# Kernel tuning notes

Hardware: AMD Instinct MI355X
Metric: run time of the kernel (lower is better)

The kernel has to match this reference:

```python
import jax, jax.numpy as jnp
import numpy as np
import math

H = 1024      # hidden_size
NH = 16       # num_heads
HD = H // NH  # head_dim
B, S = 4, 2048

def setup_inputs() -> dict:
    key = jax.random.key(0)
    ks = jax.random.split(key, 10)
    sc = 1.0 / math.sqrt(H)
    return {
        "hidden_states": jax.random.normal(ks[0], (B, S, H), dtype=jnp.float32),
        "attention_mask": jnp.ones((B, S), dtype=jnp.int32),
        "Wq": jax.random.normal(ks[1], (H, H), dtype=jnp.float32) * sc,
        "bq": jnp.zeros((H,), dtype=jnp.float32),
        "Wk": jax.random.normal(ks[2], (H, H), dtype=jnp.float32) * sc,
        "bk": jnp.zeros((H,), dtype=jnp.float32),
        "Wv": jax.random.normal(ks[3], (H, H), dtype=jnp.float32) * sc,
        "bv": jnp.zeros((H,), dtype=jnp.float32),
        "Wo": jax.random.normal(ks[4], (H, H), dtype=jnp.float32) * sc,
        "bo": jnp.zeros((H,), dtype=jnp.float32),
        "bias_correction": jnp.zeros((NH,), dtype=jnp.float32),
    }

def reference(hidden_states, attention_mask, Wq, bq, Wk, bk, Wv, bv, Wo, bo, bias_correction):
    b, s, h = hidden_states.shape
    def heads(x):  # [b,s,h] -> [b,nh,s,hd]
        return x.reshape(b, s, NH, HD).transpose(0, 2, 1, 3)
    Q = heads(hidden_states @ Wq.T + bq)
    K = heads(hidden_states @ Wk.T + bk)
    V = heads(hidden_states @ Wv.T + bv)
    scores = jnp.einsum('bhqd,bhkd->bhqk', Q, K) / math.sqrt(HD)
    scores = scores - bias_correction[None, :, None, None]
    mask = attention_mask[:, None, None, :]  # [b,1,1,s]
    scores = jnp.where(mask == 0, jnp.float32(-1e9), scores)
    attention_probs = jax.nn.softmax(scores, axis=-1)
    # dropout is identity in eval / deterministic reference
    context = jnp.einsum('bhqk,bhkd->bhqd', attention_probs, V)
    context = context.transpose(0, 2, 1, 3).reshape(b, s, h)
    output = context @ Wo.T + bo
    return (output, attention_probs)
```

## Files before the change

kernel.cpp:

```cpp
#include <hip/hip_runtime.h>
#include <stdint.h>

typedef unsigned short u16;
typedef __attribute__((ext_vector_type(8))) short short8;
typedef __attribute__((ext_vector_type(4))) float f32x4;

typedef __attribute__((address_space(1))) const unsigned int as1_uint;
typedef __attribute__((address_space(3))) unsigned int as3_uint;

#define MFMA16(a, b, c) __builtin_amdgcn_mfma_f32_16x16x32_bf16((a), (b), (c), 0, 0, 0)

__device__ __forceinline__ u16 f2bf(float f) {
  unsigned u = __float_as_uint(f);
  u += 0x7fffu + ((u >> 16) & 1u);
  return (u16)(u >> 16);
}

__global__ void cvt_kernel(const float* __restrict__ in, u16* __restrict__ out, int n4) {
  int i = blockIdx.x * blockDim.x + threadIdx.x;
  int stride = gridDim.x * blockDim.x;
  for (; i < n4; i += stride) {
    float4 v = ((const float4*)in)[i];
    ushort4 o;
    o.x = f2bf(v.x); o.y = f2bf(v.y); o.z = f2bf(v.z); o.w = f2bf(v.w);
    ((ushort4*)out)[i] = o;
  }
}

template <int MODE>
__global__ __launch_bounds__(256, 2) void gemm_bt(
    const u16* __restrict__ A, const u16* __restrict__ Bm,
    const float* __restrict__ bias, void* __restrict__ outp) {
  constexpr int K = 1024;
  constexpr int NK = K / 32;
  __shared__ u16 Asm[2][128][32];
  __shared__ u16 Bsm[2][128][32];
  const int tid = threadIdx.x;
  const int w = tid >> 6, l = tid & 63;
  const int tileM = blockIdx.x * 128, tileN = blockIdx.y * 128;
  const int lr = l >> 2;
  const int lk = (l & 3) * 8;

  f32x4 zero = {0.f, 0.f, 0.f, 0.f};
  f32x4 acc[4][4];
#pragma unroll
  for (int i = 0; i < 4; ++i)
#pragma unroll
    for (int j = 0; j < 4; ++j) acc[i][j] = zero;

  const int wm = (w >> 1) * 64, wn = (w & 1) * 64;
  const int fr = l & 15, fk = (l >> 4) * 8;

  auto stage = [&](int buf, int k0) {
#pragma unroll
    for (int j = 0; j < 2; ++j) {
      const int r0 = (j * 4 + w) * 16;
      const u16* srcA = A + (size_t)(tileM + r0 + lr) * K + (k0 + lk);
      __builtin_amdgcn_global_load_lds((as1_uint*)srcA, (as3_uint*)&Asm[buf][r0][0], 16, 0, 0);
      const u16* srcB = Bm + (size_t)(tileN + r0 + lr) * K + (k0 + lk);
      __builtin_amdgcn_global_load_lds((as1_uint*)srcB, (as3_uint*)&Bsm[buf][r0][0], 16, 0, 0);
    }
  };

  stage(0, 0);
  for (int ks = 0; ks < NK; ++ks) {
    const int buf = ks & 1;
    __syncthreads();
    if (ks + 1 < NK) stage(buf ^ 1, (ks + 1) * 32);
    short8 af[4], bfr[4];
#pragma unroll
    for (int i = 0; i < 4; ++i) af[i] = *(const short8*)&Asm[buf][wm + i * 16 + fr][fk];
#pragma unroll
    for (int j = 0; j < 4; ++j) bfr[j] = *(const short8*)&Bsm[buf][wn + j * 16 + fr][fk];
#pragma unroll
    for (int i = 0; i < 4; ++i)
#pragma unroll
      for (int j = 0; j < 4; ++j) acc[i][j] = MFMA16(af[i], bfr[j], acc[i][j]);
  }

  const int fg = (l >> 4) * 4;
#pragma unroll
  for (int i = 0; i < 4; ++i)
#pragma unroll
    for (int j = 0; j < 4; ++j) {
      const int row0 = tileM + wm + i * 16 + fg;
      const int col = tileN + wn + j * 16 + fr;
      const float bval = bias[col];
      if (MODE == 3) {
        float* out = (float*)outp;
#pragma unroll
        for (int r = 0; r < 4; ++r)
          out[(size_t)(row0 + r) * 1024 + col] = acc[i][j][r] + bval;
      } else if (MODE == 2) {
        u16* out = (u16*)outp;
        const int bb = row0 >> 11, s = row0 & 2047;
        const int hh = col >> 6, d = col & 63;
        const int q = (s >> 2) & 7;
        const int pos = (q < 4) ? (2 * q) : (2 * (q - 4) + 1);
        const int sp = (s & ~31) | (pos << 2);
        ushort4 v;
        v.x = f2bf(acc[i][j][0] + bval);
        v.y = f2bf(acc[i][j][1] + bval);
        v.z = f2bf(acc[i][j][2] + bval);
        v.w = f2bf(acc[i][j][3] + bval);
        *(ushort4*)&out[((size_t)(bb * 16 + hh) * 64 + d) * 2048 + sp] = v;
      } else {
        u16* out = (u16*)outp;
#pragma unroll
        for (int r = 0; r < 4; ++r) {
          const int row = row0 + r;
          const int bb = row >> 11, s = row & 2047;
          const int hh = col >> 6, d = col & 63;
          out[((size_t)(bb * 16 + hh) * 2048 + s) * 64 + d] = f2bf(acc[i][j][r] + bval);
        }
      }
    }
}

#define VWAIT0() asm volatile("s_waitcnt vmcnt(0)" ::: "memory")
#define VWAIT4() asm volatile("s_waitcnt vmcnt(4)" ::: "memory")
#define LWAIT0() asm volatile("s_waitcnt lgkmcnt(0)" ::: "memory")
#define BAR() asm volatile("s_barrier" ::: "memory")

__global__ __launch_bounds__(256, 3) void attn_kernel(
    const u16* __restrict__ Qb, const u16* __restrict__ Kb,
    const u16* __restrict__ VTb, const int* __restrict__ amask,
    float* __restrict__ probs, u16* __restrict__ ctx) {
  __shared__ u16 Kb2[2][4096];
  __shared__ u16 Vb2[2][4096];
  __shared__ float stg[4][1088];
  __shared__ unsigned long long mbits[32];
  const int tid = threadIdx.x;
  const int w = tid >> 6, l = tid & 63;
  const int L0 = blockIdx.x;
  const int swz = (L0 & 7) * 256 + (L0 >> 3);
  const int bh = swz >> 5, qt = swz & 31;
  const int b = bh >> 4, h = bh & 15;
  const int qw = qt * 64 + w * 16;
  const u16* Qp = Qb + ((size_t)bh * 2048 + qw) * 64;
  const u16* Kp = Kb + (size_t)bh * 2048 * 64;
  const u16* Vp = VTb + (size_t)bh * 64 * 2048;
  const int* mrow = amask + b * 2048;
  const int fr = l & 15, fg8 = (l >> 4) * 8, fg4 = (l >> 4) * 4;
  const int cd = l >> 4;
  float* stw = stg[w];

  f32x4 zero = {0.f, 0.f, 0.f, 0.f};
  short8 aq0 = *(const short8*)&Qp[fr * 64 + fg8];
  short8 aq1 = *(const short8*)&Qp[fr * 64 + 32 + fg8];

  auto stageK = [&](int buf, int kt) {
#pragma unroll
    for (int i = 0; i < 2; ++i) {
      const int Lc = tid + i * 256;
      const int row = Lc >> 3, cs = Lc & 7;
      const int c = cs ^ (row & 7);
      const u16* src = Kp + (size_t)(kt * 64 + row) * 64 + c * 8;
      __builtin_amdgcn_global_load_lds((as1_uint*)src, (as3_uint*)&Kb2[buf][Lc * 8], 16, 0, 0);
    }
  };
  auto stageV = [&](int buf, int kt) {
#pragma unroll
    for (int i = 0; i < 2; ++i) {
      const int Lc = tid + i * 256;
      const int row = Lc >> 3, cs = Lc & 7;
      const int c = cs ^ (row & 7);
      const u16* src = Vp + (size_t)row * 2048 + kt * 64 + c * 8;
      __builtin_amdgcn_global_load_lds((as1_uint*)src, (as3_uint*)&Vb2[buf][Lc * 8], 16, 0, 0);
    }
  };

#pragma unroll
  for (int i = 0; i < 8; ++i) {
    const int mv = mrow[tid + i * 256];
    const unsigned long long bal = __ballot(mv != 0);
    if (l == 0) mbits[i * 4 + w] = bal;
  }
  stageK(0, 0);
  LWAIT0();
  VWAIT0();
  BAR();

  float sa0 = 0.f, sa1 = 0.f, sa2 = 0.f, sa3 = 0.f;
  for (int kt = 0; kt < 32; ++kt) {
    const int buf = kt & 1;
    if (kt + 1 < 32) stageK(buf ^ 1, kt + 1);
    const unsigned long long mw = mbits[kt];
#pragma unroll
    for (int s = 0; s < 4; ++s) {
      const int r = s * 16 + fr;
      const int c0 = cd ^ (r & 7), c1 = (4 + cd) ^ (r & 7);
      short8 k0 = *(const short8*)&Kb2[buf][r * 64 + c0 * 8];
      short8 k1 = *(const short8*)&Kb2[buf][r * 64 + c1 * 8];
      f32x4 a = zero;
      a = MFMA16(k0, aq0, a);
      a = MFMA16(k1, aq1, a);
      const unsigned mb = (unsigned)(mw >> (s * 16 + fg4)) & 0xFu;
      const float e0 = (mb & 1u) ? __expf(a[0] * 0.125f) : 0.f;
      const float e1 = (mb & 2u) ? __expf(a[1] * 0.125f) : 0.f;
      const float e2 = (mb & 4u) ? __expf(a[2] * 0.125f) : 0.f;
      const float e3 = (mb & 8u) ? __expf(a[3] * 0.125f) : 0.f;
      const float es = (e0 + e1) + (e2 + e3);
      if (s == 0) sa0 += es;
      else if (s == 1) sa1 += es;
      else if (s == 2) sa2 += es;
      else sa3 += es;
    }
    if (kt + 1 < 32) { VWAIT0(); BAR(); }
  }
  float S = (sa0 + sa1) + (sa2 + sa3);
  S += __shfl_xor(S, 16, 64);
  S += __shfl_xor(S, 32, 64);
  const float inv = 1.0f / S;

  f32x4 acc4[4];
#pragma unroll
  for (int jd = 0; jd < 4; ++jd) acc4[jd] = zero;

  stageK(0, 0);
  stageV(0, 0);
  VWAIT0();
  BAR();
  for (int kt = 0; kt < 32; ++kt) {
    const int buf = kt & 1;
    if (kt + 1 < 32) { stageK(buf ^ 1, kt + 1); stageV(buf ^ 1, kt + 1); }
    const unsigned long long mw = mbits[kt];
    float p[4][4];
#pragma unroll
    for (int s = 0; s < 4; ++s) {
      const int r = s * 16 + fr;
      const int c0 = cd ^ (r & 7), c1 = (4 + cd) ^ (r & 7);
      short8 k0 = *(const short8*)&Kb2[buf][r * 64 + c0 * 8];
      short8 k1 = *(const short8*)&Kb2[buf][r * 64 + c1 * 8];
      f32x4 a = zero;
      a = MFMA16(k0, aq0, a);
      a = MFMA16(k1, aq1, a);
      const unsigned mb = (unsigned)(mw >> (s * 16 + fg4)) & 0xFu;
      p[s][0] = (mb & 1u) ? __expf(a[0] * 0.125f) * inv : 0.f;
      p[s][1] = (mb & 2u) ? __expf(a[1] * 0.125f) * inv : 0.f;
      p[s][2] = (mb & 4u) ? __expf(a[2] * 0.125f) * inv : 0.f;
      p[s][3] = (mb & 8u) ? __expf(a[3] * 0.125f) * inv : 0.f;
      f32x4 pv = {p[s][0], p[s][1], p[s][2], p[s][3]};
      *(f32x4*)&stw[fr * 68 + s * 16 + fg4] = pv;
    }
#pragma unroll
    for (int m = 0; m < 2; ++m) {
      short8 pb;
      pb[0] = (short)f2bf(p[2 * m][0]); pb[1] = (short)f2bf(p[2 * m][1]);
      pb[2] = (short)f2bf(p[2 * m][2]); pb[3] = (short)f2bf(p[2 * m][3]);
      pb[4] = (short)f2bf(p[2 * m + 1][0]); pb[5] = (short)f2bf(p[2 * m + 1][1]);
      pb[6] = (short)f2bf(p[2 * m + 1][2]); pb[7] = (short)f2bf(p[2 * m + 1][3]);
#pragma unroll
      for (int jd = 0; jd < 4; ++jd) {
        const int ch = (m * 4 + cd) ^ (fr & 7);
        short8 av = *(const short8*)&Vb2[buf][(jd * 16 + fr) * 64 + ch * 8];
        acc4[jd] = MFMA16(av, pb, acc4[jd]);
      }
    }
    float* pbase = probs + ((size_t)bh * 2048 + qw) * 2048 + kt * 64;
#pragma unroll
    for (int e = 0; e < 4; ++e) {
      const int row = e * 4 + cd;
      const f32x4 v = *(const f32x4*)&stw[row * 68 + fr * 4];
      __builtin_nontemporal_store(v, (f32x4*)&pbase[(size_t)row * 2048 + fr * 4]);
    }
    if (kt + 1 < 32) { VWAIT4(); BAR(); }
  }

  __syncthreads();
#pragma unroll
  for (int jd = 0; jd < 4; ++jd)
    *(f32x4*)&stw[fr * 68 + jd * 16 + fg4] = acc4[jd];
  __syncthreads();
#pragma unroll
  for (int e = 0; e < 4; ++e) {
    const int row = e * 4 + cd;
    const float4 v = *(const float4*)&stw[row * 68 + fr * 4];
    ushort4 o;
    o.x = f2bf(v.x); o.y = f2bf(v.y); o.z = f2bf(v.z); o.w = f2bf(v.w);
    *(ushort4*)&ctx[((size_t)b * 2048 + qw + row) * 1024 + h * 64 + fr * 4] = o;
  }
}

extern "C" void kernel_launch(void* const* d_in, const int* in_sizes, int n_in,
                              void* d_out, int out_size, void* d_ws, size_t ws_size,
                              hipStream_t stream) {
  const float* hs = (const float*)d_in[0];
  const int* amask = (const int*)d_in[1];
  const float* Wq = (const float*)d_in[2];
  const float* bq = (const float*)d_in[3];
  const float* Wk = (const float*)d_in[4];
  const float* bk = (const float*)d_in[5];
  const float* Wv = (const float*)d_in[6];
  const float* bv = (const float*)d_in[7];
  const float* Wo = (const float*)d_in[8];
  const float* bo = (const float*)d_in[9];
  float* out = (float*)d_out;
  float* probs = out + (size_t)4 * 2048 * 1024;

  char* ws = (char*)d_ws;
  u16* hsb = (u16*)(ws + 0);
  u16* wqb = (u16*)(ws + 16777216);
  u16* wkb = (u16*)(ws + 18874368);
  u16* wvb = (u16*)(ws + 20971520);
  u16* wob = (u16*)(ws + 23068672);
  u16* Qb  = (u16*)(ws + 25165824);
  u16* Kb  = (u16*)(ws + 41943040);
  u16* VTb = (u16*)(ws + 58720256);
  u16* ctx = (u16*)(ws + 75497472);

  cvt_kernel<<<2048, 256, 0, stream>>>(hs, hsb, 8388608 / 4);
  cvt_kernel<<<1024, 256, 0, stream>>>(Wq, wqb, 1048576 / 4);
  cvt_kernel<<<1024, 256, 0, stream>>>(Wk, wkb, 1048576 / 4);
  cvt_kernel<<<1024, 256, 0, stream>>>(Wv, wvb, 1048576 / 4);
  cvt_kernel<<<1024, 256, 0, stream>>>(Wo, wob, 1048576 / 4);

  dim3 gg(64, 8);
  gemm_bt<0><<<gg, 256, 0, stream>>>(hsb, wqb, bq, (void*)Qb);
  gemm_bt<1><<<gg, 256, 0, stream>>>(hsb, wkb, bk, (void*)Kb);
  gemm_bt<2><<<gg, 256, 0, stream>>>(hsb, wvb, bv, (void*)VTb);

  attn_kernel<<<2048, 256, 0, stream>>>(Qb, Kb, VTb, amask, probs, ctx);

  gemm_bt<3><<<gg, 256, 0, stream>>>(ctx, wob, bo, d_out);
}
```

Baseline: 387.8 us.

## Merge conversion launches and fuse Q/K/V GEMMs into one launch

The five fp32-to-bf16 conversion launches become a single grid-stride kernel that picks source and destination by index. The three Q/K/V projection GEMMs become one launch with a 64x24 grid, choosing weight, bias and output layout from blockIdx.y. This removes launch gaps and tail effects, and gives 1536 blocks to fill the GPU instead of 512 per launch. Separately, the attention kernel's launch bound goes from 3 to 4 blocks per SM, which may force register spills.

```diff
diff --git a/kernel.cpp b/kernel.cpp
--- a/kernel.cpp
+++ b/kernel.cpp
@@ -16,28 +16,49 @@
   return (u16)(u >> 16);
 }
 
-__global__ void cvt_kernel(const float* __restrict__ in, u16* __restrict__ out, int n4) {
+__global__ void cvt_all(const float* __restrict__ hs, const float* __restrict__ wq,
+                        const float* __restrict__ wk, const float* __restrict__ wv,
+                        const float* __restrict__ wo, u16* __restrict__ hsb,
+                        u16* __restrict__ wqb, u16* __restrict__ wkb,
+                        u16* __restrict__ wvb, u16* __restrict__ wob) {
   int i = blockIdx.x * blockDim.x + threadIdx.x;
-  int stride = gridDim.x * blockDim.x;
-  for (; i < n4; i += stride) {
-    float4 v = ((const float4*)in)[i];
+  const int stride = gridDim.x * blockDim.x;
+  for (; i < 3145728; i += stride) {
+    const float* src;
+    u16* dst;
+    int off;
+    if (i < 2097152) {
+      src = hs; dst = hsb; off = i;
+    } else {
+      const int j = i - 2097152;
+      const int sel = j >> 18;
+      off = j & 262143;
+      src = (sel == 0) ? wq : (sel == 1) ? wk : (sel == 2) ? wv : wo;
+      dst = (sel == 0) ? wqb : (sel == 1) ? wkb : (sel == 2) ? wvb : wob;
+    }
+    const float4 v = ((const float4*)src)[off];
     ushort4 o;
     o.x = f2bf(v.x); o.y = f2bf(v.y); o.z = f2bf(v.z); o.w = f2bf(v.w);
-    ((ushort4*)out)[i] = o;
-  }
-}
-
-template <int MODE>
-__global__ __launch_bounds__(256, 2) void gemm_bt(
-    const u16* __restrict__ A, const u16* __restrict__ Bm,
-    const float* __restrict__ bias, void* __restrict__ outp) {
+    ((ushort4*)dst)[off] = o;
+  }
+}
+
+__global__ __launch_bounds__(256, 2) void gemm_qkv(
+    const u16* __restrict__ A, const u16* __restrict__ Wqm,
+    const u16* __restrict__ Wkm, const u16* __restrict__ Wvm,
+    const float* __restrict__ bq, const float* __restrict__ bk,
+    const float* __restrict__ bv, u16* __restrict__ Qo, u16* __restrict__ Ko,
+    u16* __restrict__ Vo) {
   constexpr int K = 1024;
   constexpr int NK = K / 32;
   __shared__ u16 Asm[2][128][32];
   __shared__ u16 Bsm[2][128][32];
   const int tid = threadIdx.x;
   const int w = tid >> 6, l = tid & 63;
-  const int tileM = blockIdx.x * 128, tileN = blockIdx.y * 128;
+  const int sel = blockIdx.y >> 3;
+  const u16* Bm = (sel == 0) ? Wqm : (sel == 1) ? Wkm : Wvm;
+  const float* bias = (sel == 0) ? bq : (sel == 1) ? bk : bv;
+  const int tileM = blockIdx.x * 128, tileN = (blockIdx.y & 7) * 128;
   const int lr = l >> 2;
   const int lk = (l & 3) * 8;
 
@@ -86,13 +107,7 @@
       const int row0 = tileM + wm + i * 16 + fg;
       const int col = tileN + wn + j * 16 + fr;
       const float bval = bias[col];
-      if (MODE == 3) {
-        float* out = (float*)outp;
-#pragma unroll
-        for (int r = 0; r < 4; ++r)
-          out[(size_t)(row0 + r) * 1024 + col] = acc[i][j][r] + bval;
-      } else if (MODE == 2) {
-        u16* out = (u16*)outp;
+      if (sel == 2) {
         const int bb = row0 >> 11, s = row0 & 2047;
         const int hh = col >> 6, d = col & 63;
         const int q = (s >> 2) & 7;
@@ -103,9 +118,9 @@
         v.y = f2bf(acc[i][j][1] + bval);
         v.z = f2bf(acc[i][j][2] + bval);
         v.w = f2bf(acc[i][j][3] + bval);
-        *(ushort4*)&out[((size_t)(bb * 16 + hh) * 64 + d) * 2048 + sp] = v;
+        *(ushort4*)&Vo[((size_t)(bb * 16 + hh) * 64 + d) * 2048 + sp] = v;
       } else {
-        u16* out = (u16*)outp;
+        u16* out = (sel == 0) ? Qo : Ko;
 #pragma unroll
         for (int r = 0; r < 4; ++r) {
           const int row = row0 + r;
@@ -117,12 +132,76 @@
     }
 }
 
+__global__ __launch_bounds__(256, 2) void gemm_o(
+    const u16* __restrict__ A, const u16* __restrict__ Bm,
+    const float* __restrict__ bias, float* __restrict__ out) {
+  constexpr int K = 1024;
+  constexpr int NK = K / 32;
+  __shared__ u16 Asm[2][128][32];
+  __shared__ u16 Bsm[2][128][32];
+  const int tid = threadIdx.x;
+  const int w = tid >> 6, l = tid & 63;
+  const int tileM = blockIdx.x * 128, tileN = blockIdx.y * 128;
+  const int lr = l >> 2;
+  const int lk = (l & 3) * 8;
+
+  f32x4 zero = {0.f, 0.f, 0.f, 0.f};
+  f32x4 acc[4][4];
+#pragma unroll
+  for (int i = 0; i < 4; ++i)
+#pragma unroll
+    for (int j = 0; j < 4; ++j) acc[i][j] = zero;
+
+  const int wm = (w >> 1) * 64, wn = (w & 1) * 64;
+  const int fr = l & 15, fk = (l >> 4) * 8;
+
+  auto stage = [&](int buf, int k0) {
+#pragma unroll
+    for (int j = 0; j < 2; ++j) {
+      const int r0 = (j * 4 + w) * 16;
+      const u16* srcA = A + (size_t)(tileM + r0 + lr) * K + (k0 + lk);
+      __builtin_amdgcn_global_load_lds((as1_uint*)srcA, (as3_uint*)&Asm[buf][r0][0], 16, 0, 0);
+      const u16* srcB = Bm + (size_t)(tileN + r0 + lr) * K + (k0 + lk);
+      __builtin_amdgcn_global_load_lds((as1_uint*)srcB, (as3_uint*)&Bsm[buf][r0][0], 16, 0, 0);
+    }
+  };
+
+  stage(0, 0);
+  for (int ks = 0; ks < NK; ++ks) {
+    const int buf = ks & 1;
+    __syncthreads();
+    if (ks + 1 < NK) stage(buf ^ 1, (ks + 1) * 32);
+    short8 af[4], bfr[4];
+#pragma unroll
+    for (int i = 0; i < 4; ++i) af[i] = *(const short8*)&Asm[buf][wm + i * 16 + fr][fk];
+#pragma unroll
+    for (int j = 0; j < 4; ++j) bfr[j] = *(const short8*)&Bsm[buf][wn + j * 16 + fr][fk];
+#pragma unroll
+    for (int i = 0; i < 4; ++i)
+#pragma unroll
+      for (int j = 0; j < 4; ++j) acc[i][j] = MFMA16(af[i], bfr[j], acc[i][j]);
+  }
+
+  const int fg = (l >> 4) * 4;
+#pragma unroll
+  for (int i = 0; i < 4; ++i)
+#pragma unroll
+    for (int j = 0; j < 4; ++j) {
+      const int row0 = tileM + wm + i * 16 + fg;
+      const int col = tileN + wn + j * 16 + fr;
+      const float bval = bias[col];
+#pragma unroll
+      for (int r = 0; r < 4; ++r)
+        out[(size_t)(row0 + r) * 1024 + col] = acc[i][j][r] + bval;
+    }
+}
+
 #define VWAIT0() asm volatile("s_waitcnt vmcnt(0)" ::: "memory")
 #define VWAIT4() asm volatile("s_waitcnt vmcnt(4)" ::: "memory")
 #define LWAIT0() asm volatile("s_waitcnt lgkmcnt(0)" ::: "memory")
 #define BAR() asm volatile("s_barrier" ::: "memory")
 
-__global__ __launch_bounds__(256, 3) void attn_kernel(
+__global__ __launch_bounds__(256, 4) void attn_kernel(
     const u16* __restrict__ Qb, const u16* __restrict__ Kb,
     const u16* __restrict__ VTb, const int* __restrict__ amask,
     float* __restrict__ probs, u16* __restrict__ ctx) {
@@ -309,18 +388,11 @@
   u16* VTb = (u16*)(ws + 58720256);
   u16* ctx = (u16*)(ws + 75497472);
 
-  cvt_kernel<<<2048, 256, 0, stream>>>(hs, hsb, 8388608 / 4);
-  cvt_kernel<<<1024, 256, 0, stream>>>(Wq, wqb, 1048576 / 4);
-  cvt_kernel<<<1024, 256, 0, stream>>>(Wk, wkb, 1048576 / 4);
-  cvt_kernel<<<1024, 256, 0, stream>>>(Wv, wvb, 1048576 / 4);
-  cvt_kernel<<<1024, 256, 0, stream>>>(Wo, wob, 1048576 / 4);
-
-  dim3 gg(64, 8);
-  gemm_bt<0><<<gg, 256, 0, stream>>>(hsb, wqb, bq, (void*)Qb);
-  gemm_bt<1><<<gg, 256, 0, stream>>>(hsb, wkb, bk, (void*)Kb);
-  gemm_bt<2><<<gg, 256, 0, stream>>>(hsb, wvb, bv, (void*)VTb);
+  cvt_all<<<2048, 256, 0, stream>>>(hs, Wq, Wk, Wv, Wo, hsb, wqb, wkb, wvb, wob);
+
+  gemm_qkv<<<dim3(64, 24), 256, 0, stream>>>(hsb, wqb, wkb, wvb, bq, bk, bv, Qb, Kb, VTb);
 
   attn_kernel<<<2048, 256, 0, stream>>>(Qb, Kb, VTb, amask, probs, ctx);
 
-  gemm_bt<3><<<gg, 256, 0, stream>>>(ctx, wob, bo, d_out);
-}
+  gemm_o<<<dim3(64, 8), 256, 0, stream>>>(ctx, wob, bo, out);
+}
```

Result: slower. 396.9 us (+2.4%).
